# Kernel optimization log

Hardware: AMD Instinct MI355X
Metric: run time of the kernel (lower is better)

The kernel has to match this reference:

```python
import jax, jax.numpy as jnp
import numpy as np


def setup_inputs() -> dict:
    key = jax.random.key(0)
    k0, k1, k2, k3 = jax.random.split(key, 4)
    T, H, I, E = 2048, 2048, 5632, 8
    return {
        "hidden_states": jax.random.normal(k0, (T, H), dtype=jnp.float32),
        "gate_w": jax.random.normal(k1, (E, H), dtype=jnp.float32) * 0.02,
        "w1": jax.random.normal(k2, (E, 2 * I, H), dtype=jnp.float32) * 0.02,
        "w2": jax.random.normal(k3, (E, H, I), dtype=jnp.float32) * 0.02,
        "top_k": 2,
    }


def reference(hidden_states, gate_w, w1, w2, top_k):
    # hidden_states: [T, H]; gate_w: [E, H]; w1: [E, 2I, H]; w2: [E, H, I]
    T = hidden_states.shape[0]
    E = w1.shape[0]
    router_logits = hidden_states @ gate_w.T                    # [T, E]
    probs = jax.nn.softmax(router_logits, axis=-1)
    topk_w, topk_idx = jax.lax.top_k(probs, top_k)              # [T, k]
    # renormalize=False in fused_moe: use raw softmax top-k weights.
    # Dense combine matrix C[t, e] = weight of expert e for token t (0 if unrouted).
    combine = jnp.zeros((T, E), dtype=probs.dtype)
    combine = combine.at[jnp.arange(T)[:, None], topk_idx].add(topk_w)
    out = jnp.zeros_like(hidden_states)
    for e in range(E):  # small fixed expert loop
        gate_up = hidden_states @ w1[e].T                       # [T, 2I]
        g, u = jnp.split(gate_up, 2, axis=-1)
        h = jax.nn.silu(g) * u                                  # SiluAndMul
        out = out + combine[:, e:e + 1] * (h @ w2[e].T)         # [T, H]
    return out
```

## Files before the change

kernel.cpp:

```cpp
#include <hip/hip_runtime.h>
#include <hip/hip_bf16.h>

typedef __bf16 bf16_t;
typedef __bf16 bf16x4 __attribute__((ext_vector_type(4)));
typedef __bf16 bf16x8 __attribute__((ext_vector_type(8)));
typedef float  f32x4  __attribute__((ext_vector_type(4)));

constexpr int T_ = 2048, H_ = 2048, I_ = 5632, E_ = 8, S_ = T_ * 2;

constexpr size_t OFF_HB    = 0;
constexpr size_t OFF_HOUT  = OFF_HB    + (size_t)T_ * H_ * 2;
constexpr size_t OFF_DPART = OFF_HOUT  + (size_t)S_ * I_ * 2;
constexpr size_t OFF_TOS   = OFF_DPART + (size_t)S_ * H_ * 4;
constexpr size_t OFF_SOT   = OFF_TOS   + (size_t)S_ * 4;
constexpr size_t OFF_TKI   = OFF_SOT   + (size_t)S_ * 4;
constexpr size_t OFF_TKW   = OFF_TKI   + (size_t)S_ * 4;
constexpr size_t OFF_CNT   = OFF_TKW   + (size_t)S_ * 4;
constexpr size_t OFF_OFFS  = OFF_CNT   + 64;
constexpr size_t OFF_CUR   = OFF_OFFS  + 64;

__device__ __forceinline__ void gload16(const void* g, void* l) {
  __builtin_amdgcn_global_load_lds(
      (const __attribute__((address_space(1))) void*)g,
      (__attribute__((address_space(3))) void*)l, 16, 0, 0);
}

__device__ __forceinline__ void gld4(f32x4& d, const float* p) {
  asm volatile("global_load_dwordx4 %0, %1, off" : "=&v"(d) : "v"(p) : "memory");
}

__device__ __forceinline__ bf16x8 cvt8(f32x4 a, f32x4 b) {
  bf16x8 r;
  r[0]=(bf16_t)a[0]; r[1]=(bf16_t)a[1]; r[2]=(bf16_t)a[2]; r[3]=(bf16_t)a[3];
  r[4]=(bf16_t)b[0]; r[5]=(bf16_t)b[1]; r[6]=(bf16_t)b[2]; r[7]=(bf16_t)b[3];
  return r;
}
__device__ __forceinline__ bf16x4 cvt4v(f32x4 a) {
  bf16x4 r; r[0]=(bf16_t)a[0]; r[1]=(bf16_t)a[1]; r[2]=(bf16_t)a[2]; r[3]=(bf16_t)a[3];
  return r;
}

#define SBAR() do { __builtin_amdgcn_s_barrier(); __builtin_amdgcn_sched_barrier(0); } while (0)
#define WAITV(N) do { asm volatile("s_waitcnt vmcnt(" #N ")" ::: "memory"); \
                      __builtin_amdgcn_sched_barrier(0); } while (0)
#define WAITVL(N) do { asm volatile("s_waitcnt vmcnt(" #N ") lgkmcnt(0)" ::: "memory"); \
                       __builtin_amdgcn_sched_barrier(0); } while (0)

__global__ __launch_bounds__(256)
void router_kernel(const float* __restrict__ hs, const float* __restrict__ gw,
                   int* __restrict__ tki, float* __restrict__ tkw,
                   int* __restrict__ counts, bf16_t* __restrict__ hb)
{
  const int t = blockIdx.x;
  const int tid = threadIdx.x;
  const int lane = tid & 63, wid = tid >> 6;
  const float* hrow = hs + (size_t)t * H_;
  const int c0 = tid * 8;
  float4 h0 = *(const float4*)(hrow + c0);
  float4 h1 = *(const float4*)(hrow + c0 + 4);
  bf16x8 hv;
  hv[0]=(bf16_t)h0.x; hv[1]=(bf16_t)h0.y; hv[2]=(bf16_t)h0.z; hv[3]=(bf16_t)h0.w;
  hv[4]=(bf16_t)h1.x; hv[5]=(bf16_t)h1.y; hv[6]=(bf16_t)h1.z; hv[7]=(bf16_t)h1.w;
  *(bf16x8*)(hb + (size_t)t * H_ + c0) = hv;

  float acc[E_];
  #pragma unroll
  for (int e = 0; e < E_; ++e) {
    const float* g = gw + (size_t)e * H_ + c0;
    float4 g0 = *(const float4*)(g);
    float4 g1 = *(const float4*)(g + 4);
    acc[e] = h0.x*g0.x + h0.y*g0.y + h0.z*g0.z + h0.w*g0.w
           + h1.x*g1.x + h1.y*g1.y + h1.z*g1.z + h1.w*g1.w;
  }
  #pragma unroll
  for (int e = 0; e < E_; ++e)
    #pragma unroll
    for (int o = 32; o > 0; o >>= 1)
      acc[e] += __shfl_down(acc[e], o);
  __shared__ float red[4][E_];
  if (lane == 0)
    #pragma unroll
    for (int e = 0; e < E_; ++e) red[wid][e] = acc[e];
  __syncthreads();
  if (tid == 0) {
    float l[E_];
    #pragma unroll
    for (int e = 0; e < E_; ++e) l[e] = red[0][e] + red[1][e] + red[2][e] + red[3][e];
    float m = l[0];
    #pragma unroll
    for (int e = 1; e < E_; ++e) m = fmaxf(m, l[e]);
    float p[E_]; float s = 0.f;
    #pragma unroll
    for (int e = 0; e < E_; ++e) { p[e] = __expf(l[e] - m); s += p[e]; }
    int i1 = 0;
    #pragma unroll
    for (int e = 1; e < E_; ++e) if (l[e] > l[i1]) i1 = e;
    int i2 = (i1 == 0) ? 1 : 0;
    #pragma unroll
    for (int e = 0; e < E_; ++e) if (e != i1 && l[e] > l[i2]) i2 = e;
    tki[2*t] = i1; tki[2*t+1] = i2;
    tkw[2*t] = p[i1] / s; tkw[2*t+1] = p[i2] / s;
    atomicAdd(&counts[i1], 1);
    atomicAdd(&counts[i2], 1);
  }
}

__global__ void scan_kernel(const int* __restrict__ counts, const int* __restrict__ tki,
                            int* __restrict__ offs, int* __restrict__ cursor,
                            int* __restrict__ tos, int* __restrict__ sot)
{
  if (threadIdx.x == 0) {
    int run = 0;
    for (int e = 0; e < E_; ++e) { offs[e] = run; cursor[e] = run; run += counts[e]; }
  }
  __syncthreads();
  for (int t = threadIdx.x; t < T_; t += blockDim.x) {
    #pragma unroll
    for (int k = 0; k < 2; ++k) {
      int e = tki[2*t + k];
      int s = atomicAdd(&cursor[e], 1);
      tos[s] = t;
      sot[2*t + k] = s;
    }
  }
}

constexpr int G1_BUF = 16384 + 8192;

__global__ __launch_bounds__(512, 4)
void gemm1_kernel(const bf16_t* __restrict__ hb, const float* __restrict__ w1,
                  const int* __restrict__ tos, const int* __restrict__ offs,
                  const int* __restrict__ counts, bf16_t* __restrict__ hout)
{
  const int bid = blockIdx.x;
  const int e   = bid & 7;
  const int idx = bid >> 3;
  const int mt  = idx & 3;
  const int nt  = idx >> 2;

  const int cnt = counts[e];
  const int m0 = mt * 256;
  if (m0 >= cnt) return;
  const int off = offs[e];
  const int n0 = nt * 64;

  const float* Wg = w1 + (size_t)e * (2 * (size_t)I_ * H_) + (size_t)n0 * H_;

  __shared__ char smem[2 * G1_BUF];

  const int tid = threadIdx.x;
  const int lane = tid & 63, wid = tid >> 6;
  const int wm = wid >> 1, wn = wid & 1;
  const int l15 = lane & 15, l4 = lane >> 4;

  const bf16_t* agp[2]; int aoff[2];
  #pragma unroll
  for (int i = 0; i < 2; ++i) {
    int q = wid * 2 + i;
    int w = (lane & 7) ^ ((lane >> 3) & 7);
    int row = 2 * (q * 8 + (lane >> 3)) + (w >> 2);
    int slot = off + m0 + row, mx = off + cnt - 1;
    if (slot > mx) slot = mx;
    agp[i]  = hb + (size_t)tos[slot] * H_ + (w & 3) * 8;
    aoff[i] = q * 1024;
  }
  auto stageA = [&](int b, int t) {
    char* ab = smem + b * G1_BUF;
    #pragma unroll
    for (int i = 0; i < 2; ++i) gload16(agp[i] + t * 32, ab + aoff[i]);
  };

  const int bp = tid >> 3, bw = (tid & 7) ^ (bp & 7);
  const int bn = 2 * bp + (bw >> 2);
  const size_t brow = (bn < 64) ? (size_t)bn : (size_t)(I_ + bn - 64);
  const float* bsrc = Wg + brow * H_ + (bw & 3) * 8;

  f32x4 b0x, b0y, b1x, b1y;

  f32x4 accg[4][2], accu[4][2];
  #pragma unroll
  for (int mi = 0; mi < 4; ++mi)
    #pragma unroll
    for (int ni = 0; ni < 2; ++ni) {
      accg[mi][ni] = f32x4{0.f,0.f,0.f,0.f};
      accu[mi][ni] = f32x4{0.f,0.f,0.f,0.f};
    }

  const int phys = ((((l15 & 1) << 2) | l4) ^ ((l15 >> 1) & 7)) * 16;

  auto compute = [&](int b) {
    const char* ab = smem + b * G1_BUF;
    const char* bb = ab + 16384;
    bf16x8 bgf[2], buf2[2];
    #pragma unroll
    for (int ni = 0; ni < 2; ++ni) {
      int pb = wn * 16 + ni * 8 + (l15 >> 1);
      bgf[ni]  = *(const bf16x8*)(bb + pb * 128 + phys);
      buf2[ni] = *(const bf16x8*)(bb + (pb + 32) * 128 + phys);
    }
    #pragma unroll
    for (int mi = 0; mi < 4; ++mi) {
      int pr = wm * 32 + mi * 8 + (l15 >> 1);
      bf16x8 af = *(const bf16x8*)(ab + pr * 128 + phys);
      accg[mi][0] = __builtin_amdgcn_mfma_f32_16x16x32_bf16(af, bgf[0],  accg[mi][0], 0, 0, 0);
      accg[mi][1] = __builtin_amdgcn_mfma_f32_16x16x32_bf16(af, bgf[1],  accg[mi][1], 0, 0, 0);
      accu[mi][0] = __builtin_amdgcn_mfma_f32_16x16x32_bf16(af, buf2[0], accu[mi][0], 0, 0, 0);
      accu[mi][1] = __builtin_amdgcn_mfma_f32_16x16x32_bf16(af, buf2[1], accu[mi][1], 0, 0, 0);
    }
  };

  constexpr int NK = H_ / 32;
  int cur = 0;

  stageA(0, 0);
  gld4(b0x, bsrc);      gld4(b0y, bsrc + 4);
  gld4(b1x, bsrc + 32); gld4(b1y, bsrc + 36);
  WAITV(2);
  *(bf16x8*)(smem + 16384 + tid * 16) = cvt8(b0x, b0y);
  asm volatile("s_waitcnt lgkmcnt(0)" ::: "memory");
  SBAR();

  auto body = [&](int t, f32x4& lx, f32x4& ly, f32x4& wx, f32x4& wy) {
    stageA(cur ^ 1, t + 1);
    gld4(lx, bsrc + (t + 2) * 32);
    gld4(ly, bsrc + (t + 2) * 32 + 4);
    compute(cur);
    WAITV(4);
    *(bf16x8*)(smem + (cur ^ 1) * G1_BUF + 16384 + tid * 16) = cvt8(wx, wy);
    WAITVL(2);
    SBAR();
    cur ^= 1;
  };
  for (int t = 0; t < NK - 2; t += 2) {
    body(t,     b0x, b0y, b1x, b1y);
    body(t + 1, b1x, b1y, b0x, b0y);
  }
  stageA(cur ^ 1, NK - 1);
  compute(cur);
  WAITV(2);
  *(bf16x8*)(smem + (cur ^ 1) * G1_BUF + 16384 + tid * 16) = cvt8(b1x, b1y);
  WAITVL(0);
  SBAR();
  cur ^= 1;
  compute(cur);

  #pragma unroll
  for (int mi = 0; mi < 4; ++mi)
    #pragma unroll
    for (int ni = 0; ni < 2; ++ni)
      #pragma unroll
      for (int j = 0; j < 4; ++j) {
        int rel = wm*64 + mi*16 + l4*4 + j;
        if (m0 + rel < cnt) {
          int col = n0 + wn*32 + ni*16 + l15;
          float g = accg[mi][ni][j];
          float u = accu[mi][ni][j];
          float hvv = (g / (1.0f + __expf(-g))) * u;
          hout[(size_t)(off + m0 + rel) * I_ + col] = (bf16_t)hvv;
        }
      }
}

constexpr int G2_BUF = 16384 + 4096;

__global__ __launch_bounds__(512, 4)
void gemm2_kernel(const bf16_t* __restrict__ hbuf, const float* __restrict__ w2,
                  const int* __restrict__ offs, const int* __restrict__ counts,
                  float* __restrict__ dpart)
{
  const int bid = blockIdx.x;
  const int e   = bid & 7;
  const int idx = bid >> 3;
  const int mt  = idx & 3;
  const int nt  = idx >> 2;

  const int cnt = counts[e];
  const int m0 = mt * 256;
  if (m0 >= cnt) return;
  const int off = offs[e];
  const int n0 = nt * 64;
  const float* W = w2 + (size_t)e * ((size_t)H_ * I_) + (size_t)n0 * I_;

  __shared__ char smem[2 * G2_BUF];

  const int tid = threadIdx.x;
  const int lane = tid & 63, wid = tid >> 6;
  const int wm = wid >> 1, wn = wid & 1;
  const int l15 = lane & 15, l4 = lane >> 4;

  const bf16_t* agp[2]; int aoff[2];
  #pragma unroll
  for (int i = 0; i < 2; ++i) {
    int q = wid * 2 + i;
    int w = (lane & 7) ^ ((lane >> 3) & 7);
    int row = 2 * (q * 8 + (lane >> 3)) + (w >> 2);
    int slot = off + m0 + row, mx = off + cnt - 1;
    if (slot > mx) slot = mx;
    agp[i]  = hbuf + (size_t)slot * I_ + (w & 3) * 8;
    aoff[i] = q * 1024;
  }
  auto stageA = [&](int b, int t) {
    char* ab = smem + b * G2_BUF;
    #pragma unroll
    for (int i = 0; i < 2; ++i) gload16(agp[i] + t * 32, ab + aoff[i]);
  };

  const int s2 = tid >> 1, h2 = tid & 1;
  const int p2 = s2 >> 3, w2s = (s2 & 7) ^ (p2 & 7);
  const int bn2 = 2 * p2 + (w2s >> 2);
  const float* bsrc = W + (size_t)bn2 * I_ + (w2s & 3) * 8 + h2 * 4;
  const int bldsoff = 16384 + s2 * 16 + h2 * 8;

  f32x4 b0, b1;

  f32x4 acc[4][2];
  #pragma unroll
  for (int mi = 0; mi < 4; ++mi)
    #pragma unroll
    for (int ni = 0; ni < 2; ++ni) acc[mi][ni] = f32x4{0.f,0.f,0.f,0.f};

  const int phys = ((((l15 & 1) << 2) | l4) ^ ((l15 >> 1) & 7)) * 16;

  auto compute = [&](int b) {
    const char* ab = smem + b * G2_BUF;
    const char* bb = ab + 16384;
    bf16x8 bf[2];
    #pragma unroll
    for (int ni = 0; ni < 2; ++ni) {
      int pb = wn * 16 + ni * 8 + (l15 >> 1);
      bf[ni] = *(const bf16x8*)(bb + pb * 128 + phys);
    }
    #pragma unroll
    for (int mi = 0; mi < 4; ++mi) {
      int pr = wm * 32 + mi * 8 + (l15 >> 1);
      bf16x8 af = *(const bf16x8*)(ab + pr * 128 + phys);
      acc[mi][0] = __builtin_amdgcn_mfma_f32_16x16x32_bf16(af, bf[0], acc[mi][0], 0, 0, 0);
      acc[mi][1] = __builtin_amdgcn_mfma_f32_16x16x32_bf16(af, bf[1], acc[mi][1], 0, 0, 0);
    }
  };

  constexpr int NK = I_ / 32;
  int cur = 0;

  stageA(0, 0);
  gld4(b0, bsrc);
  gld4(b1, bsrc + 32);
  WAITV(1);
  *(bf16x4*)(smem + bldsoff) = cvt4v(b0);
  asm volatile("s_waitcnt lgkmcnt(0)" ::: "memory");
  SBAR();

  auto body = [&](int t, f32x4& lx, f32x4& wx) {
    stageA(cur ^ 1, t + 1);
    gld4(lx, bsrc + (t + 2) * 32);
    compute(cur);
    WAITV(3);
    *(bf16x4*)(smem + (cur ^ 1) * G2_BUF + bldsoff) = cvt4v(wx);
    WAITVL(1);
    SBAR();
    cur ^= 1;
  };
  for (int t = 0; t < NK - 2; t += 2) {
    body(t,     b0, b1);
    body(t + 1, b1, b0);
  }
  stageA(cur ^ 1, NK - 1);
  compute(cur);
  WAITV(2);
  *(bf16x4*)(smem + (cur ^ 1) * G2_BUF + bldsoff) = cvt4v(b1);
  WAITVL(0);
  SBAR();
  cur ^= 1;
  compute(cur);

  #pragma unroll
  for (int mi = 0; mi < 4; ++mi)
    #pragma unroll
    for (int ni = 0; ni < 2; ++ni)
      #pragma unroll
      for (int j = 0; j < 4; ++j) {
        int rel = wm*64 + mi*16 + l4*4 + j;
        if (m0 + rel < cnt) {
          int col = n0 + wn*32 + ni*16 + l15;
          dpart[(size_t)(off + m0 + rel) * H_ + col] = acc[mi][ni][j];
        }
      }
}

__global__ __launch_bounds__(256)
void combine_kernel(const float* __restrict__ dpart, const int* __restrict__ sot,
                    const float* __restrict__ tkw, float* __restrict__ out)
{
  int idx = blockIdx.x * 256 + threadIdx.x;
  int t = idx >> 9;
  int c = (idx & 511) * 4;
  float wA = tkw[2*t], wB = tkw[2*t+1];
  int sA = sot[2*t], sB = sot[2*t+1];
  float4 a = *(const float4*)(dpart + (size_t)sA * H_ + c);
  float4 b = *(const float4*)(dpart + (size_t)sB * H_ + c);
  float4 o;
  o.x = wA*a.x + wB*b.x; o.y = wA*a.y + wB*b.y;
  o.z = wA*a.z + wB*b.z; o.w = wA*a.w + wB*b.w;
  *(float4*)(out + (size_t)t * H_ + c) = o;
}

extern "C" void kernel_launch(void* const* d_in, const int* in_sizes, int n_in,
                              void* d_out, int out_size, void* d_ws, size_t ws_size,
                              hipStream_t stream) {
  const float* hs = (const float*)d_in[0];
  const float* gw = (const float*)d_in[1];
  const float* w1 = (const float*)d_in[2];
  const float* w2 = (const float*)d_in[3];
  float* out = (float*)d_out;
  char* ws = (char*)d_ws;

  bf16_t* hb    = (bf16_t*)(ws + OFF_HB);
  bf16_t* hout  = (bf16_t*)(ws + OFF_HOUT);
  float*  dpart = (float*) (ws + OFF_DPART);
  int*    tos   = (int*)   (ws + OFF_TOS);
  int*    sot   = (int*)   (ws + OFF_SOT);
  int*    tki   = (int*)   (ws + OFF_TKI);
  float*  tkw   = (float*) (ws + OFF_TKW);
  int*    cnt   = (int*)   (ws + OFF_CNT);
  int*    offp  = (int*)   (ws + OFF_OFFS);
  int*    curp  = (int*)   (ws + OFF_CUR);

  hipMemsetAsync(ws + OFF_CNT, 0, 64, stream);

  router_kernel<<<T_, 256, 0, stream>>>(hs, gw, tki, tkw, cnt, hb);
  scan_kernel<<<1, 256, 0, stream>>>(cnt, tki, offp, curp, tos, sot);
  gemm1_kernel<<<4 * (2 * I_ / 128) * E_, 512, 0, stream>>>(hb, w1, tos, offp, cnt, hout);
  gemm2_kernel<<<4 * (H_ / 64) * E_, 512, 0, stream>>>(hout, w2, offp, cnt, dpart);
  combine_kernel<<<(T_ * H_ / 4) / 256, 256, 0, stream>>>(dpart, sot, tkw, out);
}
```

Measured before the change: 1.055 ms.

## Triple-buffer A tiles, pre-gather routed tokens, and coalesce fp32 weight loads

Adds a gather kernel that copies routed token rows into a contiguous per-slot bf16 buffer, so the first GEMM reads A rows directly instead of through a tos indirection. Both expert GEMMs move from a double-buffered to a triple-buffered A stage, with prefetch two K-steps ahead. B weight loads are remapped so each thread reads contiguous fp32 segments per row, which are converted and written to swizzled LDS offsets. This aims for deeper latency hiding and more coalesced weight reads. The cost is more LDS per block, which may reduce occupancy, plus an extra kernel launch and an extra pass over the gathered activations.

```diff
diff --git a/kernel.cpp b/kernel.cpp
--- a/kernel.cpp
+++ b/kernel.cpp
@@ -18,6 +18,7 @@
 constexpr size_t OFF_CNT   = OFF_TKW   + (size_t)S_ * 4;
 constexpr size_t OFF_OFFS  = OFF_CNT   + 64;
 constexpr size_t OFF_CUR   = OFF_OFFS  + 64;
+constexpr size_t OFF_HG    = OFF_CUR   + 64;
 
 __device__ __forceinline__ void gload16(const void* g, void* l) {
   __builtin_amdgcn_global_load_lds(
@@ -29,12 +30,6 @@
   asm volatile("global_load_dwordx4 %0, %1, off" : "=&v"(d) : "v"(p) : "memory");
 }
 
-__device__ __forceinline__ bf16x8 cvt8(f32x4 a, f32x4 b) {
-  bf16x8 r;
-  r[0]=(bf16_t)a[0]; r[1]=(bf16_t)a[1]; r[2]=(bf16_t)a[2]; r[3]=(bf16_t)a[3];
-  r[4]=(bf16_t)b[0]; r[5]=(bf16_t)b[1]; r[6]=(bf16_t)b[2]; r[7]=(bf16_t)b[3];
-  return r;
-}
 __device__ __forceinline__ bf16x4 cvt4v(f32x4 a) {
   bf16x4 r; r[0]=(bf16_t)a[0]; r[1]=(bf16_t)a[1]; r[2]=(bf16_t)a[2]; r[3]=(bf16_t)a[3];
   return r;
@@ -43,8 +38,8 @@
 #define SBAR() do { __builtin_amdgcn_s_barrier(); __builtin_amdgcn_sched_barrier(0); } while (0)
 #define WAITV(N) do { asm volatile("s_waitcnt vmcnt(" #N ")" ::: "memory"); \
                       __builtin_amdgcn_sched_barrier(0); } while (0)
-#define WAITVL(N) do { asm volatile("s_waitcnt vmcnt(" #N ") lgkmcnt(0)" ::: "memory"); \
-                       __builtin_amdgcn_sched_barrier(0); } while (0)
+#define WAITL0() do { asm volatile("s_waitcnt lgkmcnt(0)" ::: "memory"); \
+                      __builtin_amdgcn_sched_barrier(0); } while (0)
 
 __global__ __launch_bounds__(256)
 void router_kernel(const float* __restrict__ hs, const float* __restrict__ gw,
@@ -125,12 +120,23 @@
   }
 }
 
-constexpr int G1_BUF = 16384 + 8192;
+__global__ __launch_bounds__(256)
+void gather_kernel(const bf16_t* __restrict__ hb, const int* __restrict__ tos,
+                   bf16_t* __restrict__ hg)
+{
+  const int slot = blockIdx.x;
+  const int tok  = tos[slot];
+  const int c = threadIdx.x * 8;
+  *(bf16x8*)(hg + (size_t)slot * H_ + c) = *(const bf16x8*)(hb + (size_t)tok * H_ + c);
+}
+
+constexpr int G1_ABUF = 16384, G1_BBUF = 8192;
+constexpr int G1_BBASE = 3 * G1_ABUF;
 
 __global__ __launch_bounds__(512, 4)
-void gemm1_kernel(const bf16_t* __restrict__ hb, const float* __restrict__ w1,
-                  const int* __restrict__ tos, const int* __restrict__ offs,
-                  const int* __restrict__ counts, bf16_t* __restrict__ hout)
+void gemm1_kernel(const bf16_t* __restrict__ hg, const float* __restrict__ w1,
+                  const int* __restrict__ offs, const int* __restrict__ counts,
+                  bf16_t* __restrict__ hout)
 {
   const int bid = blockIdx.x;
   const int e   = bid & 7;
@@ -146,7 +152,7 @@
 
   const float* Wg = w1 + (size_t)e * (2 * (size_t)I_ * H_) + (size_t)n0 * H_;
 
-  __shared__ char smem[2 * G1_BUF];
+  __shared__ char smem[3 * G1_ABUF + 2 * G1_BBUF];
 
   const int tid = threadIdx.x;
   const int lane = tid & 63, wid = tid >> 6;
@@ -161,21 +167,26 @@
     int row = 2 * (q * 8 + (lane >> 3)) + (w >> 2);
     int slot = off + m0 + row, mx = off + cnt - 1;
     if (slot > mx) slot = mx;
-    agp[i]  = hb + (size_t)tos[slot] * H_ + (w & 3) * 8;
+    agp[i]  = hg + (size_t)slot * H_ + (w & 3) * 8;
     aoff[i] = q * 1024;
   }
-  auto stageA = [&](int b, int t) {
-    char* ab = smem + b * G1_BUF;
-    #pragma unroll
-    for (int i = 0; i < 2; ++i) gload16(agp[i] + t * 32, ab + aoff[i]);
-  };
-
-  const int bp = tid >> 3, bw = (tid & 7) ^ (bp & 7);
-  const int bn = 2 * bp + (bw >> 2);
-  const size_t brow = (bn < 64) ? (size_t)bn : (size_t)(I_ + bn - 64);
-  const float* bsrc = Wg + brow * H_ + (bw & 3) * 8;
-
-  f32x4 b0x, b0y, b1x, b1y;
+  auto stageA = [&](int ab, int t) {
+    char* p = smem + ab * G1_ABUF;
+    #pragma unroll
+    for (int i = 0; i < 2; ++i) gload16(agp[i] + t * 32, p + aoff[i]);
+  };
+
+  const int brow = tid >> 3, bseg = tid & 7;
+  const float* bgsrc = Wg + (size_t)brow * H_ + bseg * 4;
+  const float* busrc = Wg + (size_t)(I_ + brow) * H_ + bseg * 4;
+  int gOff, uOff;
+  {
+    int ng = brow, nu = 64 + brow;
+    int wg_ = (ng & 1) * 4 + (bseg >> 1), wu_ = (nu & 1) * 4 + (bseg >> 1);
+    gOff = (ng >> 1) * 128 + (wg_ ^ ((ng >> 1) & 7)) * 16 + (bseg & 1) * 8;
+    uOff = (nu >> 1) * 128 + (wu_ ^ ((nu >> 1) & 7)) * 16 + (bseg & 1) * 8;
+  }
+  f32x4 b0g, b0u, b1g, b1u;
 
   f32x4 accg[4][2], accu[4][2];
   #pragma unroll
@@ -188,61 +199,67 @@
 
   const int phys = ((((l15 & 1) << 2) | l4) ^ ((l15 >> 1) & 7)) * 16;
 
-  auto compute = [&](int b) {
-    const char* ab = smem + b * G1_BUF;
-    const char* bb = ab + 16384;
+  auto compute = [&](int ab, int blds) {
+    const char* ap = smem + ab * G1_ABUF;
+    const char* bp2 = smem + G1_BBASE + blds * G1_BBUF;
     bf16x8 bgf[2], buf2[2];
     #pragma unroll
     for (int ni = 0; ni < 2; ++ni) {
       int pb = wn * 16 + ni * 8 + (l15 >> 1);
-      bgf[ni]  = *(const bf16x8*)(bb + pb * 128 + phys);
-      buf2[ni] = *(const bf16x8*)(bb + (pb + 32) * 128 + phys);
+      bgf[ni]  = *(const bf16x8*)(bp2 + pb * 128 + phys);
+      buf2[ni] = *(const bf16x8*)(bp2 + (pb + 32) * 128 + phys);
     }
     #pragma unroll
     for (int mi = 0; mi < 4; ++mi) {
       int pr = wm * 32 + mi * 8 + (l15 >> 1);
-      bf16x8 af = *(const bf16x8*)(ab + pr * 128 + phys);
+      bf16x8 af = *(const bf16x8*)(ap + pr * 128 + phys);
       accg[mi][0] = __builtin_amdgcn_mfma_f32_16x16x32_bf16(af, bgf[0],  accg[mi][0], 0, 0, 0);
       accg[mi][1] = __builtin_amdgcn_mfma_f32_16x16x32_bf16(af, bgf[1],  accg[mi][1], 0, 0, 0);
       accu[mi][0] = __builtin_amdgcn_mfma_f32_16x16x32_bf16(af, buf2[0], accu[mi][0], 0, 0, 0);
       accu[mi][1] = __builtin_amdgcn_mfma_f32_16x16x32_bf16(af, buf2[1], accu[mi][1], 0, 0, 0);
     }
   };
+  auto writeB = [&](int blds, f32x4& g, f32x4& u) {
+    char* bp2 = smem + G1_BBASE + blds * G1_BBUF;
+    *(bf16x4*)(bp2 + gOff) = cvt4v(g);
+    *(bf16x4*)(bp2 + uOff) = cvt4v(u);
+  };
 
   constexpr int NK = H_ / 32;
-  int cur = 0;
-
   stageA(0, 0);
-  gld4(b0x, bsrc);      gld4(b0y, bsrc + 4);
-  gld4(b1x, bsrc + 32); gld4(b1y, bsrc + 36);
-  WAITV(2);
-  *(bf16x8*)(smem + 16384 + tid * 16) = cvt8(b0x, b0y);
-  asm volatile("s_waitcnt lgkmcnt(0)" ::: "memory");
+  gld4(b0g, bgsrc); gld4(b0u, busrc);
+  stageA(1, 1);
+  gld4(b1g, bgsrc + 32); gld4(b1u, busrc + 32);
+  WAITV(4);
+  writeB(0, b0g, b0u);
+  WAITL0();
   SBAR();
 
-  auto body = [&](int t, f32x4& lx, f32x4& ly, f32x4& wx, f32x4& wy) {
-    stageA(cur ^ 1, t + 1);
-    gld4(lx, bsrc + (t + 2) * 32);
-    gld4(ly, bsrc + (t + 2) * 32 + 4);
-    compute(cur);
+  int aR = 0, aN = 1, aW = 2;
+  for (int t = 0; t < NK - 2; t += 2) {
+    stageA(aW, t + 2);
+    gld4(b0g, bgsrc + (t + 2) * 32); gld4(b0u, busrc + (t + 2) * 32);
+    compute(aR, 0);
     WAITV(4);
-    *(bf16x8*)(smem + (cur ^ 1) * G1_BUF + 16384 + tid * 16) = cvt8(wx, wy);
-    WAITVL(2);
+    writeB(1, b1g, b1u);
+    WAITL0();
     SBAR();
-    cur ^= 1;
-  };
-  for (int t = 0; t < NK - 2; t += 2) {
-    body(t,     b0x, b0y, b1x, b1y);
-    body(t + 1, b1x, b1y, b0x, b0y);
-  }
-  stageA(cur ^ 1, NK - 1);
-  compute(cur);
-  WAITV(2);
-  *(bf16x8*)(smem + (cur ^ 1) * G1_BUF + 16384 + tid * 16) = cvt8(b1x, b1y);
-  WAITVL(0);
+    { int tmp = aR; aR = aN; aN = aW; aW = tmp; }
+    stageA(aW, t + 3);
+    gld4(b1g, bgsrc + (t + 3) * 32); gld4(b1u, busrc + (t + 3) * 32);
+    compute(aR, 1);
+    WAITV(4);
+    writeB(0, b0g, b0u);
+    WAITL0();
+    SBAR();
+    { int tmp = aR; aR = aN; aN = aW; aW = tmp; }
+  }
+  compute(aR, 0);
+  WAITV(0);
+  writeB(1, b1g, b1u);
+  WAITL0();
   SBAR();
-  cur ^= 1;
-  compute(cur);
+  compute(aN, 1);
 
   #pragma unroll
   for (int mi = 0; mi < 4; ++mi)
@@ -261,7 +278,8 @@
       }
 }
 
-constexpr int G2_BUF = 16384 + 4096;
+constexpr int G2_ABUF = 16384, G2_BBUF = 4096;
+constexpr int G2_BBASE = 3 * G2_ABUF;
 
 __global__ __launch_bounds__(512, 4)
 void gemm2_kernel(const bf16_t* __restrict__ hbuf, const float* __restrict__ w2,
@@ -281,7 +299,7 @@
   const int n0 = nt * 64;
   const float* W = w2 + (size_t)e * ((size_t)H_ * I_) + (size_t)n0 * I_;
 
-  __shared__ char smem[2 * G2_BUF];
+  __shared__ char smem[3 * G2_ABUF + 2 * G2_BBUF];
 
   const int tid = threadIdx.x;
   const int lane = tid & 63, wid = tid >> 6;
@@ -299,18 +317,19 @@
     agp[i]  = hbuf + (size_t)slot * I_ + (w & 3) * 8;
     aoff[i] = q * 1024;
   }
-  auto stageA = [&](int b, int t) {
-    char* ab = smem + b * G2_BUF;
-    #pragma unroll
-    for (int i = 0; i < 2; ++i) gload16(agp[i] + t * 32, ab + aoff[i]);
-  };
-
-  const int s2 = tid >> 1, h2 = tid & 1;
-  const int p2 = s2 >> 3, w2s = (s2 & 7) ^ (p2 & 7);
-  const int bn2 = 2 * p2 + (w2s >> 2);
-  const float* bsrc = W + (size_t)bn2 * I_ + (w2s & 3) * 8 + h2 * 4;
-  const int bldsoff = 16384 + s2 * 16 + h2 * 8;
-
+  auto stageA = [&](int ab, int t) {
+    char* p = smem + ab * G2_ABUF;
+    #pragma unroll
+    for (int i = 0; i < 2; ++i) gload16(agp[i] + t * 32, p + aoff[i]);
+  };
+
+  const int brow = tid >> 3, bseg = tid & 7;
+  const float* bsrc = W + (size_t)brow * I_ + bseg * 4;
+  int bOff;
+  {
+    int w_ = (brow & 1) * 4 + (bseg >> 1);
+    bOff = (brow >> 1) * 128 + (w_ ^ ((brow >> 1) & 7)) * 16 + (bseg & 1) * 8;
+  }
   f32x4 b0, b1;
 
   f32x4 acc[4][2];
@@ -321,57 +340,62 @@
 
   const int phys = ((((l15 & 1) << 2) | l4) ^ ((l15 >> 1) & 7)) * 16;
 
-  auto compute = [&](int b) {
-    const char* ab = smem + b * G2_BUF;
-    const char* bb = ab + 16384;
+  auto compute = [&](int ab, int blds) {
+    const char* ap = smem + ab * G2_ABUF;
+    const char* bp2 = smem + G2_BBASE + blds * G2_BBUF;
     bf16x8 bf[2];
     #pragma unroll
     for (int ni = 0; ni < 2; ++ni) {
       int pb = wn * 16 + ni * 8 + (l15 >> 1);
-      bf[ni] = *(const bf16x8*)(bb + pb * 128 + phys);
+      bf[ni] = *(const bf16x8*)(bp2 + pb * 128 + phys);
     }
     #pragma unroll
     for (int mi = 0; mi < 4; ++mi) {
       int pr = wm * 32 + mi * 8 + (l15 >> 1);
-      bf16x8 af = *(const bf16x8*)(ab + pr * 128 + phys);
+      bf16x8 af = *(const bf16x8*)(ap + pr * 128 + phys);
       acc[mi][0] = __builtin_amdgcn_mfma_f32_16x16x32_bf16(af, bf[0], acc[mi][0], 0, 0, 0);
       acc[mi][1] = __builtin_amdgcn_mfma_f32_16x16x32_bf16(af, bf[1], acc[mi][1], 0, 0, 0);
     }
   };
+  auto writeB = [&](int blds, f32x4& v) {
+    *(bf16x4*)(smem + G2_BBASE + blds * G2_BBUF + bOff) = cvt4v(v);
+  };
 
   constexpr int NK = I_ / 32;
-  int cur = 0;
-
   stageA(0, 0);
   gld4(b0, bsrc);
+  stageA(1, 1);
   gld4(b1, bsrc + 32);
-  WAITV(1);
-  *(bf16x4*)(smem + bldsoff) = cvt4v(b0);
-  asm volatile("s_waitcnt lgkmcnt(0)" ::: "memory");
+  WAITV(3);
+  writeB(0, b0);
+  WAITL0();
   SBAR();
 
-  auto body = [&](int t, f32x4& lx, f32x4& wx) {
-    stageA(cur ^ 1, t + 1);
-    gld4(lx, bsrc + (t + 2) * 32);
-    compute(cur);
+  int aR = 0, aN = 1, aW = 2;
+  for (int t = 0; t < NK - 2; t += 2) {
+    stageA(aW, t + 2);
+    gld4(b0, bsrc + (t + 2) * 32);
+    compute(aR, 0);
     WAITV(3);
-    *(bf16x4*)(smem + (cur ^ 1) * G2_BUF + bldsoff) = cvt4v(wx);
-    WAITVL(1);
+    writeB(1, b1);
+    WAITL0();
     SBAR();
-    cur ^= 1;
-  };
-  for (int t = 0; t < NK - 2; t += 2) {
-    body(t,     b0, b1);
-    body(t + 1, b1, b0);
-  }
-  stageA(cur ^ 1, NK - 1);
-  compute(cur);
-  WAITV(2);
-  *(bf16x4*)(smem + (cur ^ 1) * G2_BUF + bldsoff) = cvt4v(b1);
-  WAITVL(0);
+    { int tmp = aR; aR = aN; aN = aW; aW = tmp; }
+    stageA(aW, t + 3);
+    gld4(b1, bsrc + (t + 3) * 32);
+    compute(aR, 1);
+    WAITV(3);
+    writeB(0, b0);
+    WAITL0();
+    SBAR();
+    { int tmp = aR; aR = aN; aN = aW; aW = tmp; }
+  }
+  compute(aR, 0);
+  WAITV(0);
+  writeB(1, b1);
+  WAITL0();
   SBAR();
-  cur ^= 1;
-  compute(cur);
+  compute(aN, 1);
 
   #pragma unroll
   for (int mi = 0; mi < 4; ++mi)
@@ -424,12 +448,14 @@
   int*    cnt   = (int*)   (ws + OFF_CNT);
   int*    offp  = (int*)   (ws + OFF_OFFS);
   int*    curp  = (int*)   (ws + OFF_CUR);
+  bf16_t* hg    = (bf16_t*)(ws + OFF_HG);
 
   hipMemsetAsync(ws + OFF_CNT, 0, 64, stream);
 
   router_kernel<<<T_, 256, 0, stream>>>(hs, gw, tki, tkw, cnt, hb);
   scan_kernel<<<1, 256, 0, stream>>>(cnt, tki, offp, curp, tos, sot);
-  gemm1_kernel<<<4 * (2 * I_ / 128) * E_, 512, 0, stream>>>(hb, w1, tos, offp, cnt, hout);
+  gather_kernel<<<S_, 256, 0, stream>>>(hb, tos, hg);
+  gemm1_kernel<<<4 * (2 * I_ / 128) * E_, 512, 0, stream>>>(hg, w1, offp, cnt, hout);
   gemm2_kernel<<<4 * (H_ / 64) * E_, 512, 0, stream>>>(hout, w2, offp, cnt, dpart);
   combine_kernel<<<(T_ * H_ / 4) / 256, 256, 0, stream>>>(dpart, sot, tkw, out);
 }
```

Result: faster. 971.7 us (-7.9%).
